# Performance work log

Hardware: AMD Instinct MI355X
Metric: run time of the kernel (lower is better)

The kernel has to match this reference:

```python
import jax, jax.numpy as jnp
import numpy as np

APREC = 8   # activation fractional bits
PPREC = 8   # parameter fractional bits
IWIDTH = 3  # integer width -> clamp to [-2**IWIDTH, 2**IWIDTH - 1]

QMAX = 2.0 ** IWIDTH - 1.0
QMIN = -(2.0 ** IWIDTH)


def quant(v, prec):
    # round to 2**-prec grid (torch.round and jnp.round both round-half-to-even)
    s = 2.0 ** prec
    return jnp.round(v * s) / s


def round_max(v):
    # the relu-chain in the source is exactly a clamp to [QMIN, QMAX]
    return jnp.clip(v, QMIN, QMAX)


def fixed_point_conv(x, w, b):
    """Quantized 'conv': each elementwise product w[j,m,p,q]*x[b,m,k+p,l+q] is
    rounded to the activation grid and clamped BEFORE summation, then bias added.
    x: [B,Cin,H,W], w: [Cout,Cin,K,K], b: [Cout].
    Loop is over the KxK fixed kernel offsets (25), fully vectorized over B/Cout/Cin/space."""
    w = quant(w, PPREC)
    b = quant(b, PPREC)
    K = w.shape[2]
    Ho = x.shape[2] - K + 1
    Wo = x.shape[3] - K + 1
    out = jnp.zeros((x.shape[0], w.shape[0], Ho, Wo), dtype=x.dtype)
    for p in range(K):
        for q in range(K):
            # [B, Cout, Cin, Ho, Wo]
            prod = x[:, None, :, p:p + Ho, q:q + Wo] * w[None, :, :, p, q, None, None]
            prod = round_max(quant(prod, APREC))
            out = out + prod.sum(axis=2)
    return out + b[None, :, None, None]


def fixed_point_fc(x, w, b):
    # x: [B, in], w: [out, in], b: [out]
    w = round_max(quant(w, PPREC))
    b = round_max(quant(b, PPREC))
    x = round_max(quant(x, APREC))
    out = x @ w.T + b[None, :]
    out = round_max(out)
    return quant(out, APREC)


def max_pool2(x):
    return jax.lax.reduce_window(x, -jnp.inf, jax.lax.max,
                                 (1, 1, 2, 2), (1, 1, 2, 2), 'VALID')


def setup_inputs() -> dict:
    key = jax.random.key(0)
    ks = jax.random.split(key, 9)
    B = 2048
    return {
        'x': jax.random.normal(ks[0], (B, 1, 28, 28), jnp.float32),
        'conv1_w': jax.random.normal(ks[1], (10, 1, 5, 5), jnp.float32) * 0.2,
        'conv1_b': jax.random.normal(ks[2], (10,), jnp.float32) * 0.1,
        'conv2_w': jax.random.normal(ks[3], (20, 10, 5, 5), jnp.float32) * 0.1,
        'conv2_b': jax.random.normal(ks[4], (20,), jnp.float32) * 0.1,
        'fc1_w': jax.random.normal(ks[5], (50, 320), jnp.float32) * 0.05,
        'fc1_b': jax.random.normal(ks[6], (50,), jnp.float32) * 0.05,
        'fc2_w': jax.random.normal(ks[7], (10, 50), jnp.float32) * 0.1,
        'fc2_b': jax.random.normal(ks[8], (10,), jnp.float32) * 0.1,
    }


def reference(x, conv1_w, conv1_b, conv2_w, conv2_b, fc1_w, fc1_b, fc2_w, fc2_b):
    x = quant(x, APREC)
    conv1_input = x
    x = fixed_point_conv(x, conv1_w, conv1_b)          # [B,10,24,24]
    x = quant(x, APREC)
    conv1_output = x
    x = jax.nn.relu(max_pool2(x))                      # [B,10,12,12]
    x = quant(x, APREC)
    conv2_input = x
    x = fixed_point_conv(x, conv2_w, conv2_b)          # [B,20,8,8]
    x = quant(x, APREC)
    conv2_output = x
    # Dropout2d / F.dropout are identity in eval mode
    x = jax.nn.relu(max_pool2(x))                      # [B,20,4,4]
    x = x.reshape(-1, 320)
    x = quant(x, APREC)
    fc1_input = x
    x = fixed_point_fc(x, fc1_w, fc1_b)                # [B,50]
    x = quant(x, APREC)
    fc1_output = x
    x = jax.nn.relu(x)
    x = quant(x, APREC)
    fc2_input = x
    x = fixed_point_fc(x, fc2_w, fc2_b)                # [B,10]
    x = quant(x, APREC)
    fc2_output = x
    logp = jax.nn.log_softmax(x, axis=1)
    return (logp, conv1_input, conv1_output, conv2_input, conv2_output,
            fc1_input, fc1_output, fc2_input, fc2_output)
```

## Files before the change

### kernel.cpp

```cpp
#include <hip/hip_runtime.h>
#include <math.h>


#define NB 2048

#define OFF_LOGP   0
#define OFF_C1IN   (OFF_LOGP  + NB*10)
#define OFF_C1OUT  (OFF_C1IN  + NB*784)
#define OFF_C2IN   (OFF_C1OUT + NB*5760)
#define OFF_C2OUT  (OFF_C2IN  + NB*1440)
#define OFF_FC1IN  (OFF_C2OUT + NB*1280)
#define OFF_FC1OUT (OFF_FC1IN + NB*320)
#define OFF_FC2IN  (OFF_FC1OUT+ NB*50)
#define OFF_FC2OUT (OFF_FC2IN + NB*50)

#define MAGIC_F 12582912.0f

__device__ __forceinline__ float clamp8(float v) {
    return __builtin_amdgcn_fmed3f(v, -8.0f, 7.0f);
}

__global__ __launch_bounds__(256, 3)
void k1_conv1(const float* __restrict__ x,
              const float* __restrict__ cw1, const float* __restrict__ cb1,
              float* __restrict__ out)
{
    __shared__ __align__(16) float s_w1[140];
    __shared__ float s_b1[5];
    __shared__ __align__(16) float s_x[784];

    const int t    = threadIdx.x;
    const int img  = blockIdx.x >> 1;
    const int half = blockIdx.x & 1;

    if (t < 125) s_w1[(t / 25) * 28 + (t % 25)] = rintf(cw1[half * 125 + t] * 256.0f);
    if (t < 5)   s_b1[t] = rintf(cb1[half * 5 + t] * 256.0f);

    const float* xg = x + (size_t)img * 784;
    float* c1in_g = out + OFF_C1IN + (size_t)img * 784;
    for (int i = t; i < 784; i += 256) {
        float v = rintf(xg[i] * 256.0f) * (1.0f / 256.0f);
        s_x[i] = v;
        if (half == 0) c1in_g[i] = v;
    }
    __syncthreads();

    if (t < 240) {
        const int co_l = t / 48;
        const int co   = half * 5 + co_l;
        const int r    = t % 48;
        const int i    = r >> 1;
        const int jh   = r & 1;

        float wreg[28];
        {
            const float* wb = s_w1 + co_l * 28;
            #pragma unroll
            for (int k = 0; k < 7; k++) {
                float4 v4 = *(const float4*)(wb + 4 * k);
                wreg[4*k] = v4.x; wreg[4*k+1] = v4.y; wreg[4*k+2] = v4.z; wreg[4*k+3] = v4.w;
            }
        }

        float acc[12];
        #pragma unroll
        for (int j = 0; j < 12; j++) acc[j] = MAGIC_F;

        #pragma unroll
        for (int p = 0; p < 5; p++) {
            float xr[16];
            const float* row = &s_x[(i + p) * 28 + 12 * jh];
            #pragma unroll
            for (int k = 0; k < 4; k++) {
                float4 v4 = *(const float4*)(row + 4 * k);
                xr[4*k] = v4.x; xr[4*k+1] = v4.y; xr[4*k+2] = v4.z; xr[4*k+3] = v4.w;
            }
            #pragma unroll
            for (int q = 0; q < 5; q++) {
                float w = wreg[p * 5 + q];
                #pragma unroll
                for (int j = 0; j < 12; j++)
                    acc[j] = fmaf(xr[q + j], w, acc[j]);
            }
        }
        const float C = MAGIC_F - s_b1[co_l];
        float v[12];
        #pragma unroll
        for (int j = 0; j < 12; j++) v[j] = (acc[j] - C) * (1.0f / 256.0f);

        float* gdst = out + OFF_C1OUT + (size_t)img * 5760 + co * 576 + i * 24 + 12 * jh;
        #pragma unroll
        for (int k = 0; k < 3; k++) {
            float4 st = { v[4*k], v[4*k+1], v[4*k+2], v[4*k+3] };
            *(float4*)(gdst + 4 * k) = st;
        }

        float m[6];
        #pragma unroll
        for (int j2 = 0; j2 < 6; j2++) m[j2] = fmaxf(v[2*j2], v[2*j2+1]);
        float pm[6];
        #pragma unroll
        for (int j2 = 0; j2 < 6; j2++) pm[j2] = __shfl_xor(m[j2], 2);

        if ((i & 1) == 0) {
            float pr[6];
            #pragma unroll
            for (int j2 = 0; j2 < 6; j2++)
                pr[j2] = fmaxf(fmaxf(m[j2], pm[j2]), 0.0f);
            float* g = out + OFF_C2IN + (size_t)img * 1440 + co * 144 + (i >> 1) * 12 + 6 * jh;
            #pragma unroll
            for (int k = 0; k < 3; k++) {
                float2 st = { pr[2*k], pr[2*k+1] };
                *(float2*)(g + 2 * k) = st;
            }
        }
    }
}

__global__ __launch_bounds__(320, 2)
void k2_rest(const float* __restrict__ cw2, const float* __restrict__ cb2,
             const float* __restrict__ fw1, const float* __restrict__ fb1,
             const float* __restrict__ fw2, const float* __restrict__ fb2,
             float* __restrict__ out)
{
    __shared__ __align__(16) float s_w2[5600];
    __shared__ float s_b2[20];
    __shared__ __align__(16) float s_p1[1440];
    __shared__ float s_p2[320];
    __shared__ float s_fc2in[50];
    __shared__ float s_fc2out[10];

    const int t   = threadIdx.x;
    const int img = blockIdx.x;

    for (int idx = t; idx < 5000; idx += 320) {
        int cc = idx / 25, q = idx % 25;
        s_w2[cc * 28 + q] = rintf(cw2[idx] * 256.0f);
    }
    if (t < 20) s_b2[t] = rintf(cb2[t] * 256.0f);

    const float* p1g = out + OFF_C2IN + (size_t)img * 1440;
    for (int i = t; i < 1440; i += 320) s_p1[i] = p1g[i];
    __syncthreads();

    const int co = t >> 4;
    const int i  = (t >> 1) & 7;
    const int jh = t & 1;

    float acc[4] = { MAGIC_F, MAGIC_F, MAGIC_F, MAGIC_F };
    for (int ci = 0; ci < 10; ci++) {
        float wreg[28];
        {
            const float* wb = s_w2 + (co * 10 + ci) * 28;
            #pragma unroll
            for (int k = 0; k < 7; k++) {
                float4 v4 = *(const float4*)(wb + 4 * k);
                wreg[4*k] = v4.x; wreg[4*k+1] = v4.y; wreg[4*k+2] = v4.z; wreg[4*k+3] = v4.w;
            }
        }
        const float* xb = s_p1 + ci * 144 + jh * 4;
        #pragma unroll
        for (int p = 0; p < 5; p++) {
            const float* row = xb + (i + p) * 12;
            float4 a4 = *(const float4*)(row);
            float4 b4 = *(const float4*)(row + 4);
            float xr[8] = { a4.x, a4.y, a4.z, a4.w, b4.x, b4.y, b4.z, b4.w };
            #pragma unroll
            for (int q = 0; q < 5; q++) {
                float w = wreg[p * 5 + q];
                #pragma unroll
                for (int j = 0; j < 4; j++)
                    acc[j] = fmaf(xr[q + j], w, acc[j]);
            }
        }
    }
    const float C2 = MAGIC_F - s_b2[co];
    float v[4];
    #pragma unroll
    for (int j = 0; j < 4; j++) v[j] = (acc[j] - C2) * (1.0f / 256.0f);

    {
        float4 st = { v[0], v[1], v[2], v[3] };
        *(float4*)(out + OFF_C2OUT + (size_t)img * 1280 + co * 64 + i * 8 + jh * 4) = st;
    }

    float m0 = fmaxf(v[0], v[1]);
    float m1 = fmaxf(v[2], v[3]);
    float pm0 = __shfl_xor(m0, 2);
    float pm1 = __shfl_xor(m1, 2);
    if ((i & 1) == 0) {
        float r0 = fmaxf(fmaxf(m0, pm0), 0.0f);
        float r1 = fmaxf(fmaxf(m1, pm1), 0.0f);
        int o = co * 16 + (i >> 1) * 4 + jh * 2;
        out[OFF_FC1IN + (size_t)img * 320 + o]     = r0;
        out[OFF_FC1IN + (size_t)img * 320 + o + 1] = r1;
        s_p2[o]     = clamp8(r0);
        s_p2[o + 1] = clamp8(r1);
    }
    __syncthreads();

    float* s_fcp = s_p1;
    if (t < 250) {
        const int j = t / 5, c = t % 5;
        const float* wr = fw1 + j * 320 + c * 64;
        const float* xr = s_p2 + c * 64;
        float s = 0.0f;
        #pragma unroll 8
        for (int k = 0; k < 64; k++) {
            float wq = clamp8(rintf(wr[k] * 256.0f) * (1.0f / 256.0f));
            s = fmaf(xr[k], wq, s);
        }
        s_fcp[t] = s;
    }
    __syncthreads();

    if (t < 50) {
        float acc1 = clamp8(rintf(fb1[t] * 256.0f) * (1.0f / 256.0f));
        #pragma unroll
        for (int c = 0; c < 5; c++) acc1 += s_fcp[t * 5 + c];
        float o1 = rintf(clamp8(acc1) * 256.0f) * (1.0f / 256.0f);
        out[OFF_FC1OUT + (size_t)img * 50 + t] = o1;
        float r = fmaxf(o1, 0.0f);
        out[OFF_FC2IN + (size_t)img * 50 + t] = r;
        s_fc2in[t] = clamp8(r);
    }
    __syncthreads();

    if (t < 10) {
        float acc2 = clamp8(rintf(fb2[t] * 256.0f) * (1.0f / 256.0f));
        const float* wr = fw2 + t * 50;
        for (int k = 0; k < 50; k++) {
            float wq = clamp8(rintf(wr[k] * 256.0f) * (1.0f / 256.0f));
            acc2 = fmaf(s_fc2in[k], wq, acc2);
        }
        float o2 = rintf(clamp8(acc2) * 256.0f) * (1.0f / 256.0f);
        out[OFF_FC2OUT + (size_t)img * 10 + t] = o2;
        s_fc2out[t] = o2;
    }
    __syncthreads();

    if (t == 0) {
        float m = s_fc2out[0];
        for (int k = 1; k < 10; k++) m = fmaxf(m, s_fc2out[k]);
        float ssum = 0.0f;
        for (int k = 0; k < 10; k++) ssum += expf(s_fc2out[k] - m);
        float lse = m + logf(ssum);
        for (int k = 0; k < 10; k++)
            out[OFF_LOGP + (size_t)img * 10 + k] = s_fc2out[k] - lse;
    }
}

extern "C" void kernel_launch(void* const* d_in, const int* in_sizes, int n_in,
                              void* d_out, int out_size, void* d_ws, size_t ws_size,
                              hipStream_t stream) {
    const float* x   = (const float*)d_in[0];
    const float* cw1 = (const float*)d_in[1];
    const float* cb1 = (const float*)d_in[2];
    const float* cw2 = (const float*)d_in[3];
    const float* cb2 = (const float*)d_in[4];
    const float* fw1 = (const float*)d_in[5];
    const float* fb1 = (const float*)d_in[6];
    const float* fw2 = (const float*)d_in[7];
    const float* fb2 = (const float*)d_in[8];
    float* o = (float*)d_out;

    k1_conv1<<<2 * NB, 256, 0, stream>>>(x, cw1, cb1, o);
    k2_rest <<<NB, 320, 0, stream>>>(cw2, cb2, fw1, fb1, fw2, fb2, o);
}
```

Baseline: 177.6 us.

## Split FC layers into separate wave-per-image kernel with prequantized transposed weights

Moves the fully connected layers and log-softmax out of the conv2 kernel into a new kernel where each 64-lane wavefront handles one image, using fc weights that block 0 of conv1 prequantizes and transposes into workspace. Conv2 blocks now process two images each, which amortizes the conv2 weight staging into shared memory. This targets the serial, poorly parallel FC tail (a single thread doing the softmax, 10 threads doing fc2) and the repeated per-block requantization of fc weights. In exchange it adds a third kernel launch, extra global round trips for the fc inputs, and a larger shared-memory footprint for conv2.

New measurement: 193.2 us. +8.8%, slower.

```diff
diff --git a/kernel.cpp b/kernel.cpp
--- a/kernel.cpp
+++ b/kernel.cpp
@@ -16,6 +16,11 @@
 
 #define MAGIC_F 12582912.0f
 
+#define WS_WT1 0
+#define WS_B1  20480
+#define WS_WT2 20544
+#define WS_B2  21344
+
 __device__ __forceinline__ float clamp8(float v) {
     return __builtin_amdgcn_fmed3f(v, -8.0f, 7.0f);
 }
@@ -23,6 +28,9 @@
 __global__ __launch_bounds__(256, 3)
 void k1_conv1(const float* __restrict__ x,
               const float* __restrict__ cw1, const float* __restrict__ cb1,
+              const float* __restrict__ fw1, const float* __restrict__ fb1,
+              const float* __restrict__ fw2, const float* __restrict__ fb2,
+              float* __restrict__ ws,
               float* __restrict__ out)
 {
     __shared__ __align__(16) float s_w1[140];
@@ -115,23 +123,35 @@
             }
         }
     }
-}
-
-__global__ __launch_bounds__(320, 2)
-void k2_rest(const float* __restrict__ cw2, const float* __restrict__ cb2,
-             const float* __restrict__ fw1, const float* __restrict__ fb1,
-             const float* __restrict__ fw2, const float* __restrict__ fb2,
-             float* __restrict__ out)
+
+    if (blockIdx.x == 0) {
+        for (int idx = t; idx < 20480; idx += 256) {
+            int k = idx >> 6, j = idx & 63;
+            float v = 0.0f;
+            if (j < 50) v = clamp8(rintf(fw1[j * 320 + k] * 256.0f) * (1.0f / 256.0f));
+            ws[WS_WT1 + idx] = v;
+        }
+        for (int idx = t; idx < 800; idx += 256) {
+            int k = idx >> 4, j = idx & 15;
+            float v = 0.0f;
+            if (j < 10) v = clamp8(rintf(fw2[j * 50 + k] * 256.0f) * (1.0f / 256.0f));
+            ws[WS_WT2 + idx] = v;
+        }
+        if (t < 64) ws[WS_B1 + t] = (t < 50) ? clamp8(rintf(fb1[t] * 256.0f) * (1.0f / 256.0f)) : 0.0f;
+        if (t < 16) ws[WS_B2 + t] = (t < 10) ? clamp8(rintf(fb2[t] * 256.0f) * (1.0f / 256.0f)) : 0.0f;
+    }
+}
+
+__global__ __launch_bounds__(320)
+void k2_conv2(const float* __restrict__ cw2, const float* __restrict__ cb2,
+              float* __restrict__ out)
 {
     __shared__ __align__(16) float s_w2[5600];
     __shared__ float s_b2[20];
-    __shared__ __align__(16) float s_p1[1440];
-    __shared__ float s_p2[320];
-    __shared__ float s_fc2in[50];
-    __shared__ float s_fc2out[10];
-
-    const int t   = threadIdx.x;
-    const int img = blockIdx.x;
+    __shared__ __align__(16) float s_p1[2 * 1440];
+
+    const int t    = threadIdx.x;
+    const int img0 = blockIdx.x * 2;
 
     for (int idx = t; idx < 5000; idx += 320) {
         int cc = idx / 25, q = idx % 25;
@@ -139,115 +159,115 @@
     }
     if (t < 20) s_b2[t] = rintf(cb2[t] * 256.0f);
 
-    const float* p1g = out + OFF_C2IN + (size_t)img * 1440;
-    for (int i = t; i < 1440; i += 320) s_p1[i] = p1g[i];
+    const float* p1g = out + OFF_C2IN + (size_t)img0 * 1440;
+    for (int i = t; i < 2880; i += 320) s_p1[i] = p1g[i];
     __syncthreads();
 
     const int co = t >> 4;
     const int i  = (t >> 1) & 7;
     const int jh = t & 1;
-
-    float acc[4] = { MAGIC_F, MAGIC_F, MAGIC_F, MAGIC_F };
-    for (int ci = 0; ci < 10; ci++) {
-        float wreg[28];
+    const float C2 = MAGIC_F - s_b2[co];
+
+    for (int im = 0; im < 2; im++) {
+        const int img = img0 + im;
+
+        float acc[4] = { MAGIC_F, MAGIC_F, MAGIC_F, MAGIC_F };
+        for (int ci = 0; ci < 10; ci++) {
+            float wreg[28];
+            {
+                const float* wb = s_w2 + (co * 10 + ci) * 28;
+                #pragma unroll
+                for (int k = 0; k < 7; k++) {
+                    float4 v4 = *(const float4*)(wb + 4 * k);
+                    wreg[4*k] = v4.x; wreg[4*k+1] = v4.y; wreg[4*k+2] = v4.z; wreg[4*k+3] = v4.w;
+                }
+            }
+            const float* xb = s_p1 + im * 1440 + ci * 144 + jh * 4;
+            #pragma unroll
+            for (int p = 0; p < 5; p++) {
+                const float* row = xb + (i + p) * 12;
+                float4 a4 = *(const float4*)(row);
+                float4 b4 = *(const float4*)(row + 4);
+                float xr[8] = { a4.x, a4.y, a4.z, a4.w, b4.x, b4.y, b4.z, b4.w };
+                #pragma unroll
+                for (int q = 0; q < 5; q++) {
+                    float w = wreg[p * 5 + q];
+                    #pragma unroll
+                    for (int j = 0; j < 4; j++)
+                        acc[j] = fmaf(xr[q + j], w, acc[j]);
+                }
+            }
+        }
+        float v[4];
+        #pragma unroll
+        for (int j = 0; j < 4; j++) v[j] = (acc[j] - C2) * (1.0f / 256.0f);
+
         {
-            const float* wb = s_w2 + (co * 10 + ci) * 28;
-            #pragma unroll
-            for (int k = 0; k < 7; k++) {
-                float4 v4 = *(const float4*)(wb + 4 * k);
-                wreg[4*k] = v4.x; wreg[4*k+1] = v4.y; wreg[4*k+2] = v4.z; wreg[4*k+3] = v4.w;
-            }
-        }
-        const float* xb = s_p1 + ci * 144 + jh * 4;
-        #pragma unroll
-        for (int p = 0; p < 5; p++) {
-            const float* row = xb + (i + p) * 12;
-            float4 a4 = *(const float4*)(row);
-            float4 b4 = *(const float4*)(row + 4);
-            float xr[8] = { a4.x, a4.y, a4.z, a4.w, b4.x, b4.y, b4.z, b4.w };
-            #pragma unroll
-            for (int q = 0; q < 5; q++) {
-                float w = wreg[p * 5 + q];
-                #pragma unroll
-                for (int j = 0; j < 4; j++)
-                    acc[j] = fmaf(xr[q + j], w, acc[j]);
-            }
-        }
-    }
-    const float C2 = MAGIC_F - s_b2[co];
-    float v[4];
+            float4 st = { v[0], v[1], v[2], v[3] };
+            *(float4*)(out + OFF_C2OUT + (size_t)img * 1280 + co * 64 + i * 8 + jh * 4) = st;
+        }
+
+        float m0 = fmaxf(v[0], v[1]);
+        float m1 = fmaxf(v[2], v[3]);
+        float pm0 = __shfl_xor(m0, 2);
+        float pm1 = __shfl_xor(m1, 2);
+        if ((i & 1) == 0) {
+            float r0 = fmaxf(fmaxf(m0, pm0), 0.0f);
+            float r1 = fmaxf(fmaxf(m1, pm1), 0.0f);
+            int o = co * 16 + (i >> 1) * 4 + jh * 2;
+            out[OFF_FC1IN + (size_t)img * 320 + o]     = r0;
+            out[OFF_FC1IN + (size_t)img * 320 + o + 1] = r1;
+        }
+    }
+}
+
+__global__ __launch_bounds__(256)
+void k3_fc(const float* __restrict__ ws, float* __restrict__ out)
+{
+    __shared__ float s_x[4][320];
+
+    const int t    = threadIdx.x;
+    const int wv   = t >> 6;
+    const int lane = t & 63;
+    const int img  = blockIdx.x * 4 + wv;
+
+    const float* xg = out + OFF_FC1IN + (size_t)img * 320;
     #pragma unroll
-    for (int j = 0; j < 4; j++) v[j] = (acc[j] - C2) * (1.0f / 256.0f);
-
-    {
-        float4 st = { v[0], v[1], v[2], v[3] };
-        *(float4*)(out + OFF_C2OUT + (size_t)img * 1280 + co * 64 + i * 8 + jh * 4) = st;
-    }
-
-    float m0 = fmaxf(v[0], v[1]);
-    float m1 = fmaxf(v[2], v[3]);
-    float pm0 = __shfl_xor(m0, 2);
-    float pm1 = __shfl_xor(m1, 2);
-    if ((i & 1) == 0) {
-        float r0 = fmaxf(fmaxf(m0, pm0), 0.0f);
-        float r1 = fmaxf(fmaxf(m1, pm1), 0.0f);
-        int o = co * 16 + (i >> 1) * 4 + jh * 2;
-        out[OFF_FC1IN + (size_t)img * 320 + o]     = r0;
-        out[OFF_FC1IN + (size_t)img * 320 + o + 1] = r1;
-        s_p2[o]     = clamp8(r0);
-        s_p2[o + 1] = clamp8(r1);
-    }
+    for (int r = 0; r < 5; r++)
+        s_x[wv][lane + 64 * r] = clamp8(xg[lane + 64 * r]);
     __syncthreads();
 
-    float* s_fcp = s_p1;
-    if (t < 250) {
-        const int j = t / 5, c = t % 5;
-        const float* wr = fw1 + j * 320 + c * 64;
-        const float* xr = s_p2 + c * 64;
-        float s = 0.0f;
-        #pragma unroll 8
-        for (int k = 0; k < 64; k++) {
-            float wq = clamp8(rintf(wr[k] * 256.0f) * (1.0f / 256.0f));
-            s = fmaf(xr[k], wq, s);
-        }
-        s_fcp[t] = s;
-    }
-    __syncthreads();
-
-    if (t < 50) {
-        float acc1 = clamp8(rintf(fb1[t] * 256.0f) * (1.0f / 256.0f));
-        #pragma unroll
-        for (int c = 0; c < 5; c++) acc1 += s_fcp[t * 5 + c];
-        float o1 = rintf(clamp8(acc1) * 256.0f) * (1.0f / 256.0f);
-        out[OFF_FC1OUT + (size_t)img * 50 + t] = o1;
-        float r = fmaxf(o1, 0.0f);
-        out[OFF_FC2IN + (size_t)img * 50 + t] = r;
-        s_fc2in[t] = clamp8(r);
-    }
-    __syncthreads();
-
-    if (t < 10) {
-        float acc2 = clamp8(rintf(fb2[t] * 256.0f) * (1.0f / 256.0f));
-        const float* wr = fw2 + t * 50;
-        for (int k = 0; k < 50; k++) {
-            float wq = clamp8(rintf(wr[k] * 256.0f) * (1.0f / 256.0f));
-            acc2 = fmaf(s_fc2in[k], wq, acc2);
-        }
-        float o2 = rintf(clamp8(acc2) * 256.0f) * (1.0f / 256.0f);
-        out[OFF_FC2OUT + (size_t)img * 10 + t] = o2;
-        s_fc2out[t] = o2;
-    }
-    __syncthreads();
-
-    if (t == 0) {
-        float m = s_fc2out[0];
-        for (int k = 1; k < 10; k++) m = fmaxf(m, s_fc2out[k]);
-        float ssum = 0.0f;
-        for (int k = 0; k < 10; k++) ssum += expf(s_fc2out[k] - m);
-        float lse = m + logf(ssum);
-        for (int k = 0; k < 10; k++)
-            out[OFF_LOGP + (size_t)img * 10 + k] = s_fc2out[k] - lse;
-    }
+    float acc = ws[WS_B1 + lane];
+    #pragma unroll 8
+    for (int k = 0; k < 320; k++)
+        acc = fmaf(s_x[wv][k], ws[WS_WT1 + k * 64 + lane], acc);
+    float o1 = rintf(clamp8(acc) * 256.0f) * (1.0f / 256.0f);
+    float r1 = fmaxf(o1, 0.0f);
+    if (lane < 50) {
+        out[OFF_FC1OUT + (size_t)img * 50 + lane] = o1;
+        out[OFF_FC2IN  + (size_t)img * 50 + lane] = r1;
+    }
+    float yc = clamp8(r1);
+
+    float acc2 = ws[WS_B2 + (lane & 15)];
+    #pragma unroll 10
+    for (int k = 0; k < 50; k++) {
+        float yk = __shfl(yc, k);
+        acc2 = fmaf(yk, ws[WS_WT2 + k * 16 + (lane & 15)], acc2);
+    }
+    float o2 = rintf(clamp8(acc2) * 256.0f) * (1.0f / 256.0f);
+    if (lane < 10) out[OFF_FC2OUT + (size_t)img * 10 + lane] = o2;
+
+    float v = (lane < 10) ? o2 : -3.0e38f;
+    #pragma unroll
+    for (int d = 1; d < 16; d <<= 1)
+        v = fmaxf(v, __shfl_xor(v, d, 16));
+    float e = (lane < 10) ? expf(o2 - v) : 0.0f;
+    #pragma unroll
+    for (int d = 1; d < 16; d <<= 1)
+        e += __shfl_xor(e, d, 16);
+    float lse = v + logf(e);
+    if (lane < 10) out[OFF_LOGP + (size_t)img * 10 + lane] = o2 - lse;
 }
 
 extern "C" void kernel_launch(void* const* d_in, const int* in_sizes, int n_in,
@@ -262,8 +282,10 @@
     const float* fb1 = (const float*)d_in[6];
     const float* fw2 = (const float*)d_in[7];
     const float* fb2 = (const float*)d_in[8];
-    float* o = (float*)d_out;
-
-    k1_conv1<<<2 * NB, 256, 0, stream>>>(x, cw1, cb1, o);
-    k2_rest <<<NB, 320, 0, stream>>>(cw2, cb2, fw1, fb1, fw2, fb2, o);
-}
+    float* o  = (float*)d_out;
+    float* ws = (float*)d_ws;
+
+    k1_conv1<<<2 * NB, 256, 0, stream>>>(x, cw1, cb1, fw1, fb1, fw2, fb2, ws, o);
+    k2_conv2<<<NB / 2, 320, 0, stream>>>(cw2, cb2, o);
+    k3_fc   <<<NB / 4, 256, 0, stream>>>(ws, o);
+}
```
